# Kernel tuning notes

Hardware: AMD Instinct MI355X
Metric: run time of the kernel (lower is better)

The kernel has to match this reference:

```python
import jax, jax.numpy as jnp
import numpy as np
from functools import partial

EPS = 1e-8

@partial(jax.custom_vjp, nondiff_argnums=(2, 3))
def ste_quantize(x, scale, clamp_min, clamp_max):
    # forward: clamp(round(x/scale), min, max); backward: grad/scale (STE)
    return jnp.clip(jnp.round(x / scale), clamp_min, clamp_max)

def _ste_fwd(x, scale, clamp_min, clamp_max):
    return ste_quantize(x, scale, clamp_min, clamp_max), scale

def _ste_bwd(clamp_min, clamp_max, scale, g):
    return (g / scale, jnp.zeros_like(scale))

ste_quantize.defvjp(_ste_fwd, _ste_bwd)


def setup_inputs() -> dict:
    key = jax.random.key(0)
    kx, kw = jax.random.split(key)
    x = jax.random.normal(kx, (4, 4096, 2048), dtype=jnp.float32)
    # nn.init.normal_(weight, mean=0.0, std=0.006)
    weight = 0.006 * jax.random.normal(kw, (2048, 2048), dtype=jnp.float32)
    return {"x": x, "weight": weight}


def reference(x, weight):
    # per-tensor ternary weight quantization: alpha = mean(|W|)
    alpha = jnp.maximum(jnp.mean(jnp.abs(weight)), EPS)
    w_q = ste_quantize(weight, alpha, -1.0, 1.0)  # (out, in), values in {-1,0,1}
    # per-token int8 activation quantization: beta = max(|x|)/127
    beta = jnp.maximum(jnp.max(jnp.abs(x), axis=-1, keepdims=True) / 127.0, EPS)  # (b,s,1)
    x_q = ste_quantize(x, beta, -127.0, 127.0)  # (b,s,in)
    # fp32 GEMM on quantized values, then dequant rescale
    y = jnp.einsum('bsi,oi->bso', x_q, w_q)
    return y * alpha * beta
```

## Files before the change

kernel.cpp:

```cpp
#include <hip/hip_runtime.h>

#define IN_DIM 2048
#define OUT_DIM 2048
#define EPS 1e-8f

#define BK 128
#define NKT (IN_DIM / BK)
#define HALF 16384

using int32x4 = __attribute__((ext_vector_type(4))) int;

__global__ __launch_bounds__(256) void absum_kernel(const float* __restrict__ w,
                                                    double* __restrict__ sum, int n4) {
    int tid = blockIdx.x * blockDim.x + threadIdx.x;
    int stride = gridDim.x * blockDim.x;
    float s = 0.f;
    for (int i = tid; i < n4; i += stride) {
        float4 v = ((const float4*)w)[i];
        s += fabsf(v.x) + fabsf(v.y) + fabsf(v.z) + fabsf(v.w);
    }
    for (int off = 32; off; off >>= 1) s += __shfl_down(s, off);
    __shared__ float wsum[4];
    int lane = threadIdx.x & 63, wave = threadIdx.x >> 6;
    if (lane == 0) wsum[wave] = s;
    __syncthreads();
    if (threadIdx.x == 0) {
        double t = (double)wsum[0] + (double)wsum[1] + (double)wsum[2] + (double)wsum[3];
        atomicAdd(sum, t);
    }
}

__global__ __launch_bounds__(256) void quantw_kernel(const float* __restrict__ w,
                                                     const double* __restrict__ sumptr,
                                                     signed char* __restrict__ wq,
                                                     float* __restrict__ alpha_out, int n4) {
    float alpha = fmaxf((float)(*sumptr * (1.0 / (double)(IN_DIM * OUT_DIM))), EPS);
    int i = blockIdx.x * blockDim.x + threadIdx.x;
    if (i == 0) *alpha_out = alpha;
    if (i >= n4) return;
    float4 v = ((const float4*)w)[i];
    char4 q;
    q.x = (signed char)fminf(fmaxf(rintf(v.x / alpha), -1.f), 1.f);
    q.y = (signed char)fminf(fmaxf(rintf(v.y / alpha), -1.f), 1.f);
    q.z = (signed char)fminf(fmaxf(rintf(v.z / alpha), -1.f), 1.f);
    q.w = (signed char)fminf(fmaxf(rintf(v.w / alpha), -1.f), 1.f);
    ((char4*)wq)[i] = q;
}

__global__ __launch_bounds__(256) void quantx_kernel(const float* __restrict__ x,
                                                     signed char* __restrict__ xq,
                                                     float* __restrict__ beta_arr,
                                                     int tokens) {
    const int tid = threadIdx.x;
    const int lane = tid & 63, wave = tid >> 6;
    __shared__ float wmax[4];
    for (int t = blockIdx.x; t < tokens; t += gridDim.x) {
        const float4* row = (const float4*)(x + (size_t)t * IN_DIM);
        float4 v0 = row[tid];
        float4 v1 = row[tid + 256];
        float m = fmaxf(fmaxf(fmaxf(fabsf(v0.x), fabsf(v0.y)), fmaxf(fabsf(v0.z), fabsf(v0.w))),
                        fmaxf(fmaxf(fabsf(v1.x), fabsf(v1.y)), fmaxf(fabsf(v1.z), fabsf(v1.w))));
        for (int off = 32; off; off >>= 1) m = fmaxf(m, __shfl_xor(m, off));
        if (lane == 0) wmax[wave] = m;
        __syncthreads();
        m = fmaxf(fmaxf(wmax[0], wmax[1]), fmaxf(wmax[2], wmax[3]));
        float beta = fmaxf(m * (1.f / 127.f), EPS);
        if (tid == 0) beta_arr[t] = beta;
        char4 q0, q1;
        q0.x = (signed char)fminf(fmaxf(rintf(v0.x / beta), -127.f), 127.f);
        q0.y = (signed char)fminf(fmaxf(rintf(v0.y / beta), -127.f), 127.f);
        q0.z = (signed char)fminf(fmaxf(rintf(v0.z / beta), -127.f), 127.f);
        q0.w = (signed char)fminf(fmaxf(rintf(v0.w / beta), -127.f), 127.f);
        q1.x = (signed char)fminf(fmaxf(rintf(v1.x / beta), -127.f), 127.f);
        q1.y = (signed char)fminf(fmaxf(rintf(v1.y / beta), -127.f), 127.f);
        q1.z = (signed char)fminf(fmaxf(rintf(v1.z / beta), -127.f), 127.f);
        q1.w = (signed char)fminf(fmaxf(rintf(v1.w / beta), -127.f), 127.f);
        char4* orow = (char4*)(xq + (size_t)t * IN_DIM);
        orow[tid] = q0;
        orow[tid + 256] = q1;
        __syncthreads();
    }
}

__device__ __forceinline__ void gll(const signed char* g, signed char* l) {
    __builtin_amdgcn_global_load_lds((const __attribute__((address_space(1))) void*)g,
        (__attribute__((address_space(3))) void*)l, 16, 0, 0);
}

#define CLUSTER(BASE, AF)                                                                      \
    __builtin_amdgcn_s_setprio(1);                                                             \
    _Pragma("unroll")                                                                          \
    for (int m_ = 0; m_ < 4; ++m_)                                                             \
        _Pragma("unroll")                                                                      \
        for (int n_ = 0; n_ < 4; ++n_)                                                         \
            acc[(BASE) + m_][n_] = __builtin_amdgcn_mfma_i32_16x16x64_i8(                      \
                AF[m_], bf[n_], acc[(BASE) + m_][n_], 0, 0, 0);                                \
    __builtin_amdgcn_s_setprio(0);

template<bool STG, bool TAIL>
__device__ __forceinline__ void ktile(int T, signed char* lds, int32x4 (&acc)[8][4],
                                      int aoff, int boff, int f0, int f1,
                                      const signed char* a0, const signed char* a1,
                                      const signed char* b0, const signed char* b1) {
    const int s = (T & 1) * HALF;
    const int d = ((T + 1) & 1) * HALF;
    const size_t ko = (size_t)(T + 1) * BK;
    int32x4 af0[4], af1[4], bf[4];

#pragma unroll
    for (int m = 0; m < 4; ++m) af0[m] = *(const int32x4*)(lds + s + aoff + m * 1024);
#pragma unroll
    for (int n = 0; n < 4; ++n) bf[n] = *(const int32x4*)(lds + 65536 + s + boff + n * 1024);
    if constexpr (STG) { gll(a0 + ko, lds + d + f0); gll(a1 + ko, lds + d + f1); }
#pragma unroll
    for (int m = 0; m < 4; ++m) af1[m] = *(const int32x4*)(lds + s + aoff + 4096 + m * 1024);
    CLUSTER(0, af0)
    if constexpr (STG) { gll(b0 + ko, lds + 65536 + d + f0); gll(b1 + ko, lds + 65536 + d + f1); }
    CLUSTER(4, af1)
    if constexpr (TAIL) asm volatile("s_waitcnt vmcnt(0)" ::: "memory");
    else                asm volatile("s_waitcnt vmcnt(4)" ::: "memory");
    __builtin_amdgcn_s_barrier();

#pragma unroll
    for (int m = 0; m < 4; ++m) af0[m] = *(const int32x4*)(lds + 32768 + s + aoff + m * 1024);
#pragma unroll
    for (int n = 0; n < 4; ++n) bf[n] = *(const int32x4*)(lds + 98304 + s + boff + n * 1024);
    if constexpr (STG) { gll(a0 + ko + 64, lds + 32768 + d + f0); gll(a1 + ko + 64, lds + 32768 + d + f1); }
#pragma unroll
    for (int m = 0; m < 4; ++m) af1[m] = *(const int32x4*)(lds + 32768 + s + aoff + 4096 + m * 1024);
    CLUSTER(0, af0)
    if constexpr (STG) { gll(b0 + ko + 64, lds + 98304 + d + f0); gll(b1 + ko + 64, lds + 98304 + d + f1); }
    CLUSTER(4, af1)
    if constexpr (!TAIL) {
        asm volatile("s_waitcnt vmcnt(4)" ::: "memory");
        __builtin_amdgcn_s_barrier();
    }
}

__global__ __launch_bounds__(512, 2) void gemm_kernel(const signed char* __restrict__ xq,
                                                      const signed char* __restrict__ wq,
                                                      const float* __restrict__ beta,
                                                      const float* __restrict__ alpha_p,
                                                      float* __restrict__ out) {
    extern __shared__ signed char lds[];
    const int tid = threadIdx.x;
    const int lane = tid & 63;
    const int wave = tid >> 6;
    const int wm = wave >> 2;
    const int wn = wave & 3;
    const int row0 = blockIdx.x * 256;
    const int col0 = blockIdx.y * 256;

    const int f0 = tid * 16;
    const int f1 = f0 + 8192;
    const int g0 = f0 >> 10, kg0 = (f0 >> 8) & 3, r0 = (f0 >> 4) & 15;
    const int g1 = f1 >> 10, kg1 = (f1 >> 8) & 3, r1 = (f1 >> 4) & 15;
    const signed char* a0 = xq + (size_t)(row0 + g0 * 16 + r0) * IN_DIM + kg0 * 16;
    const signed char* a1 = xq + (size_t)(row0 + g1 * 16 + r1) * IN_DIM + kg1 * 16;
    const signed char* b0 = wq + (size_t)(col0 + g0 * 16 + r0) * IN_DIM + kg0 * 16;
    const signed char* b1 = wq + (size_t)(col0 + g1 * 16 + r1) * IN_DIM + kg1 * 16;

    const int kr = (lane >> 4) * 256 + (lane & 15) * 16;
    const int aoff = wm * 8192 + kr;
    const int boff = wn * 4096 + kr;

    int32x4 acc[8][4] = {};

    gll(a0, lds + f0);              gll(a1, lds + f1);
    gll(b0, lds + 65536 + f0);      gll(b1, lds + 65536 + f1);
    gll(a0 + 64, lds + 32768 + f0); gll(a1 + 64, lds + 32768 + f1);
    gll(b0 + 64, lds + 98304 + f0); gll(b1 + 64, lds + 98304 + f1);
    asm volatile("s_waitcnt vmcnt(4)" ::: "memory");
    __builtin_amdgcn_s_barrier();

    for (int T = 0; T < NKT - 1; ++T)
        ktile<true, false>(T, lds, acc, aoff, boff, f0, f1, a0, a1, b0, b1);
    ktile<false, true>(NKT - 1, lds, acc, aoff, boff, f0, f1, a0, a1, b0, b1);

    const float alpha = *alpha_p;
#pragma unroll
    for (int mi = 0; mi < 8; ++mi) {
        int rbase = row0 + wm * 128 + mi * 16 + ((lane >> 4) << 2);
#pragma unroll
        for (int r = 0; r < 4; ++r) {
            int row = rbase + r;
            float scale = alpha * beta[row];
#pragma unroll
            for (int n = 0; n < 4; ++n) {
                int col = col0 + wn * 64 + n * 16 + (lane & 15);
                out[(size_t)row * OUT_DIM + col] = (float)acc[mi][n][r] * scale;
            }
        }
    }
}

extern "C" void kernel_launch(void* const* d_in, const int* in_sizes, int n_in,
                              void* d_out, int out_size, void* d_ws, size_t ws_size,
                              hipStream_t stream) {
    const float* x = (const float*)d_in[0];
    const float* w = (const float*)d_in[1];
    float* out = (float*)d_out;

    const int tokens = in_sizes[0] / IN_DIM;
    const int n_w = in_sizes[1];
    const int n_w4 = n_w / 4;

    char* ws = (char*)d_ws;
    double* d_sum = (double*)ws;
    float* d_alpha = (float*)(ws + 8);
    float* d_beta = (float*)(ws + 256);
    signed char* d_wq = (signed char*)(ws + 256 + 65536);
    signed char* d_xq = d_wq + (size_t)n_w;

    hipMemsetAsync(d_ws, 0, 16, stream);

    absum_kernel<<<1024, 256, 0, stream>>>(w, d_sum, n_w4);
    quantw_kernel<<<(n_w4 + 255) / 256, 256, 0, stream>>>(w, d_sum, d_wq, d_alpha, n_w4);
    quantx_kernel<<<2048, 256, 0, stream>>>(x, d_xq, d_beta, tokens);

    hipFuncSetAttribute((const void*)gemm_kernel,
                        hipFuncAttributeMaxDynamicSharedMemorySize, 131072);

    dim3 grid(16384 / 256, OUT_DIM / 256);
    gemm_kernel<<<grid, 512, 131072, stream>>>(d_xq, d_wq, d_beta, d_alpha, out);
}
```

Before: 152.4 us.

## Restructure int8 GEMM to 256x128 tiles with triple-buffered BK=64 pipeline

Replaces the 256x256, 512-thread, double-buffered BK=128 GEMM with a 256x128 tile on 256 threads (4 waves, each 128x64). It uses a three-slot LDS ring with BK=64, so loads are issued two tiles ahead and there is one barrier per k-step. LDS drops from 128 KB to 72 KB per block, and the grid now iterates columns fastest so blocks sharing an A row-panel run close together. The aim is better occupancy and latency hiding, at the cost of more k-iterations, halved B reuse per A tile, and more redundant A traffic across column blocks.

```diff
diff --git a/kernel.cpp b/kernel.cpp
--- a/kernel.cpp
+++ b/kernel.cpp
@@ -4,9 +4,12 @@
 #define OUT_DIM 2048
 #define EPS 1e-8f
 
-#define BK 128
-#define NKT (IN_DIM / BK)
-#define HALF 16384
+#define BM 256
+#define BN 128
+#define BK 64
+#define NT (IN_DIM / BK)
+#define SLOT 24576
+#define LDS_SZ 73728
 
 using int32x4 = __attribute__((ext_vector_type(4))) int;
 
@@ -87,57 +90,7 @@
         (__attribute__((address_space(3))) void*)l, 16, 0, 0);
 }
 
-#define CLUSTER(BASE, AF)                                                                      \
-    __builtin_amdgcn_s_setprio(1);                                                             \
-    _Pragma("unroll")                                                                          \
-    for (int m_ = 0; m_ < 4; ++m_)                                                             \
-        _Pragma("unroll")                                                                      \
-        for (int n_ = 0; n_ < 4; ++n_)                                                         \
-            acc[(BASE) + m_][n_] = __builtin_amdgcn_mfma_i32_16x16x64_i8(                      \
-                AF[m_], bf[n_], acc[(BASE) + m_][n_], 0, 0, 0);                                \
-    __builtin_amdgcn_s_setprio(0);
-
-template<bool STG, bool TAIL>
-__device__ __forceinline__ void ktile(int T, signed char* lds, int32x4 (&acc)[8][4],
-                                      int aoff, int boff, int f0, int f1,
-                                      const signed char* a0, const signed char* a1,
-                                      const signed char* b0, const signed char* b1) {
-    const int s = (T & 1) * HALF;
-    const int d = ((T + 1) & 1) * HALF;
-    const size_t ko = (size_t)(T + 1) * BK;
-    int32x4 af0[4], af1[4], bf[4];
-
-#pragma unroll
-    for (int m = 0; m < 4; ++m) af0[m] = *(const int32x4*)(lds + s + aoff + m * 1024);
-#pragma unroll
-    for (int n = 0; n < 4; ++n) bf[n] = *(const int32x4*)(lds + 65536 + s + boff + n * 1024);
-    if constexpr (STG) { gll(a0 + ko, lds + d + f0); gll(a1 + ko, lds + d + f1); }
-#pragma unroll
-    for (int m = 0; m < 4; ++m) af1[m] = *(const int32x4*)(lds + s + aoff + 4096 + m * 1024);
-    CLUSTER(0, af0)
-    if constexpr (STG) { gll(b0 + ko, lds + 65536 + d + f0); gll(b1 + ko, lds + 65536 + d + f1); }
-    CLUSTER(4, af1)
-    if constexpr (TAIL) asm volatile("s_waitcnt vmcnt(0)" ::: "memory");
-    else                asm volatile("s_waitcnt vmcnt(4)" ::: "memory");
-    __builtin_amdgcn_s_barrier();
-
-#pragma unroll
-    for (int m = 0; m < 4; ++m) af0[m] = *(const int32x4*)(lds + 32768 + s + aoff + m * 1024);
-#pragma unroll
-    for (int n = 0; n < 4; ++n) bf[n] = *(const int32x4*)(lds + 98304 + s + boff + n * 1024);
-    if constexpr (STG) { gll(a0 + ko + 64, lds + 32768 + d + f0); gll(a1 + ko + 64, lds + 32768 + d + f1); }
-#pragma unroll
-    for (int m = 0; m < 4; ++m) af1[m] = *(const int32x4*)(lds + 32768 + s + aoff + 4096 + m * 1024);
-    CLUSTER(0, af0)
-    if constexpr (STG) { gll(b0 + ko + 64, lds + 98304 + d + f0); gll(b1 + ko + 64, lds + 98304 + d + f1); }
-    CLUSTER(4, af1)
-    if constexpr (!TAIL) {
-        asm volatile("s_waitcnt vmcnt(4)" ::: "memory");
-        __builtin_amdgcn_s_barrier();
-    }
-}
-
-__global__ __launch_bounds__(512, 2) void gemm_kernel(const signed char* __restrict__ xq,
+__global__ __launch_bounds__(256, 2) void gemm_kernel(const signed char* __restrict__ xq,
                                                       const signed char* __restrict__ wq,
                                                       const float* __restrict__ beta,
                                                       const float* __restrict__ alpha_p,
@@ -146,36 +99,81 @@
     const int tid = threadIdx.x;
     const int lane = tid & 63;
     const int wave = tid >> 6;
-    const int wm = wave >> 2;
-    const int wn = wave & 3;
-    const int row0 = blockIdx.x * 256;
-    const int col0 = blockIdx.y * 256;
-
-    const int f0 = tid * 16;
-    const int f1 = f0 + 8192;
-    const int g0 = f0 >> 10, kg0 = (f0 >> 8) & 3, r0 = (f0 >> 4) & 15;
-    const int g1 = f1 >> 10, kg1 = (f1 >> 8) & 3, r1 = (f1 >> 4) & 15;
-    const signed char* a0 = xq + (size_t)(row0 + g0 * 16 + r0) * IN_DIM + kg0 * 16;
-    const signed char* a1 = xq + (size_t)(row0 + g1 * 16 + r1) * IN_DIM + kg1 * 16;
-    const signed char* b0 = wq + (size_t)(col0 + g0 * 16 + r0) * IN_DIM + kg0 * 16;
-    const signed char* b1 = wq + (size_t)(col0 + g1 * 16 + r1) * IN_DIM + kg1 * 16;
-
-    const int kr = (lane >> 4) * 256 + (lane & 15) * 16;
+    const int wm = wave >> 1;
+    const int wn = wave & 1;
+    const int col0 = blockIdx.x * BN;
+    const int row0 = blockIdx.y * BM;
+
+    const int f = tid * 16;
+    const int srow = ((tid >> 6) << 4) + (tid & 15);
+    const int skg = ((tid >> 4) & 3) << 4;
+    const signed char* aP[4];
+    const signed char* bP[2];
+#pragma unroll
+    for (int c = 0; c < 4; ++c) aP[c] = xq + (size_t)(row0 + srow + 64 * c) * IN_DIM + skg;
+#pragma unroll
+    for (int c = 0; c < 2; ++c) bP[c] = wq + (size_t)(col0 + srow + 64 * c) * IN_DIM + skg;
+
+    const int kr = ((lane >> 4) << 8) + ((lane & 15) << 4);
     const int aoff = wm * 8192 + kr;
-    const int boff = wn * 4096 + kr;
+    const int boff = 16384 + wn * 4096 + kr;
 
     int32x4 acc[8][4] = {};
 
-    gll(a0, lds + f0);              gll(a1, lds + f1);
-    gll(b0, lds + 65536 + f0);      gll(b1, lds + 65536 + f1);
-    gll(a0 + 64, lds + 32768 + f0); gll(a1 + 64, lds + 32768 + f1);
-    gll(b0 + 64, lds + 98304 + f0); gll(b1 + 64, lds + 98304 + f1);
-    asm volatile("s_waitcnt vmcnt(4)" ::: "memory");
+#pragma unroll
+    for (int c = 0; c < 4; ++c) gll(aP[c], lds + f + c * 4096);
+#pragma unroll
+    for (int c = 0; c < 2; ++c) gll(bP[c], lds + 16384 + f + c * 4096);
+#pragma unroll
+    for (int c = 0; c < 4; ++c) gll(aP[c] + BK, lds + SLOT + f + c * 4096);
+#pragma unroll
+    for (int c = 0; c < 2; ++c) gll(bP[c] + BK, lds + SLOT + 16384 + f + c * 4096);
+    asm volatile("s_waitcnt vmcnt(6)" ::: "memory");
     __builtin_amdgcn_s_barrier();
 
-    for (int T = 0; T < NKT - 1; ++T)
-        ktile<true, false>(T, lds, acc, aoff, boff, f0, f1, a0, a1, b0, b1);
-    ktile<false, true>(NKT - 1, lds, acc, aoff, boff, f0, f1, a0, a1, b0, b1);
+    int s = 0, d = 2;
+    for (int T = 0; T < NT; ++T) {
+        const signed char* ls = lds + s * SLOT;
+        signed char* ldst = lds + d * SLOT;
+        int32x4 af[8], bf[4];
+#pragma unroll
+        for (int m = 0; m < 4; ++m) af[m] = *(const int32x4*)(ls + aoff + m * 1024);
+#pragma unroll
+        for (int n = 0; n < 4; ++n) bf[n] = *(const int32x4*)(ls + boff + n * 1024);
+        if (T < NT - 2) {
+            const size_t ko = (size_t)(T + 2) * BK;
+#pragma unroll
+            for (int c = 0; c < 4; ++c) gll(aP[c] + ko, ldst + f + c * 4096);
+        }
+#pragma unroll
+        for (int m = 0; m < 4; ++m) af[4 + m] = *(const int32x4*)(ls + aoff + 4096 + m * 1024);
+        __builtin_amdgcn_s_setprio(1);
+#pragma unroll
+        for (int m = 0; m < 4; ++m)
+#pragma unroll
+            for (int n = 0; n < 4; ++n)
+                acc[m][n] = __builtin_amdgcn_mfma_i32_16x16x64_i8(af[m], bf[n], acc[m][n], 0, 0, 0);
+        __builtin_amdgcn_s_setprio(0);
+        if (T < NT - 2) {
+            const size_t ko = (size_t)(T + 2) * BK;
+#pragma unroll
+            for (int c = 0; c < 2; ++c) gll(bP[c] + ko, ldst + 16384 + f + c * 4096);
+        }
+        __builtin_amdgcn_s_setprio(1);
+#pragma unroll
+        for (int m = 0; m < 4; ++m)
+#pragma unroll
+            for (int n = 0; n < 4; ++n)
+                acc[4 + m][n] = __builtin_amdgcn_mfma_i32_16x16x64_i8(af[4 + m], bf[n], acc[4 + m][n], 0, 0, 0);
+        __builtin_amdgcn_s_setprio(0);
+        if (T < NT - 1) {
+            if (T < NT - 2) asm volatile("s_waitcnt vmcnt(6)" ::: "memory");
+            else            asm volatile("s_waitcnt vmcnt(0)" ::: "memory");
+            __builtin_amdgcn_s_barrier();
+        }
+        s = (s == 2) ? 0 : s + 1;
+        d = (d == 2) ? 0 : d + 1;
+    }
 
     const float alpha = *alpha_p;
 #pragma unroll
@@ -219,8 +217,8 @@
     quantx_kernel<<<2048, 256, 0, stream>>>(x, d_xq, d_beta, tokens);
 
     hipFuncSetAttribute((const void*)gemm_kernel,
-                        hipFuncAttributeMaxDynamicSharedMemorySize, 131072);
-
-    dim3 grid(16384 / 256, OUT_DIM / 256);
-    gemm_kernel<<<grid, 512, 131072, stream>>>(d_xq, d_wq, d_beta, d_alpha, out);
-}
+                        hipFuncAttributeMaxDynamicSharedMemorySize, LDS_SZ);
+
+    dim3 grid(OUT_DIM / BN, tokens / BM);
+    gemm_kernel<<<grid, 256, LDS_SZ, stream>>>(d_xq, d_wq, d_beta, d_alpha, out);
+}
```

After: 172.0 us. +12.8%, slower.

## Restructure int8 GEMM k-tile into barrier-synchronised LDS-load / MFMA phases

Applied to the files above, without the earlier changes.

Each half k-tile is split into two phases. Each phase loads one A fragment set, then runs a block barrier, waits for LDS reads (lgkmcnt) and places a scheduler fence before a 16-MFMA cluster. The second A fragment array is dropped, so A fragments reuse one register set. The aim is to cut register pressure and to make waves alternate between LDS-read and MFMA phases in a ping-pong style. It adds two extra block barriers per half-tile and removes the overlap of A-fragment loads with the previous MFMA cluster, which may stall the matrix pipe.

```diff
diff --git a/kernel.cpp b/kernel.cpp
--- a/kernel.cpp
+++ b/kernel.cpp
@@ -87,7 +87,12 @@
         (__attribute__((address_space(3))) void*)l, 16, 0, 0);
 }
 
-#define CLUSTER(BASE, AF)                                                                      \
+#define PRE_MFMA()                                              \
+    __builtin_amdgcn_s_barrier();                               \
+    asm volatile("s_waitcnt lgkmcnt(0)" ::: "memory");          \
+    __builtin_amdgcn_sched_barrier(0);
+
+#define MFMA16(BASE, AF)                                                                       \
     __builtin_amdgcn_s_setprio(1);                                                             \
     _Pragma("unroll")                                                                          \
     for (int m_ = 0; m_ < 4; ++m_)                                                             \
@@ -105,32 +110,40 @@
     const int s = (T & 1) * HALF;
     const int d = ((T + 1) & 1) * HALF;
     const size_t ko = (size_t)(T + 1) * BK;
-    int32x4 af0[4], af1[4], bf[4];
-
-#pragma unroll
-    for (int m = 0; m < 4; ++m) af0[m] = *(const int32x4*)(lds + s + aoff + m * 1024);
+    int32x4 af[4], bf[4];
+
+#pragma unroll
+    for (int m = 0; m < 4; ++m) af[m] = *(const int32x4*)(lds + s + aoff + m * 1024);
 #pragma unroll
     for (int n = 0; n < 4; ++n) bf[n] = *(const int32x4*)(lds + 65536 + s + boff + n * 1024);
     if constexpr (STG) { gll(a0 + ko, lds + d + f0); gll(a1 + ko, lds + d + f1); }
-#pragma unroll
-    for (int m = 0; m < 4; ++m) af1[m] = *(const int32x4*)(lds + s + aoff + 4096 + m * 1024);
-    CLUSTER(0, af0)
+    PRE_MFMA()
+    MFMA16(0, af)
+    __builtin_amdgcn_s_barrier();
+
+#pragma unroll
+    for (int m = 0; m < 4; ++m) af[m] = *(const int32x4*)(lds + s + aoff + 4096 + m * 1024);
     if constexpr (STG) { gll(b0 + ko, lds + 65536 + d + f0); gll(b1 + ko, lds + 65536 + d + f1); }
-    CLUSTER(4, af1)
+    PRE_MFMA()
+    MFMA16(4, af)
     if constexpr (TAIL) asm volatile("s_waitcnt vmcnt(0)" ::: "memory");
     else                asm volatile("s_waitcnt vmcnt(4)" ::: "memory");
     __builtin_amdgcn_s_barrier();
 
 #pragma unroll
-    for (int m = 0; m < 4; ++m) af0[m] = *(const int32x4*)(lds + 32768 + s + aoff + m * 1024);
+    for (int m = 0; m < 4; ++m) af[m] = *(const int32x4*)(lds + 32768 + s + aoff + m * 1024);
 #pragma unroll
     for (int n = 0; n < 4; ++n) bf[n] = *(const int32x4*)(lds + 98304 + s + boff + n * 1024);
     if constexpr (STG) { gll(a0 + ko + 64, lds + 32768 + d + f0); gll(a1 + ko + 64, lds + 32768 + d + f1); }
-#pragma unroll
-    for (int m = 0; m < 4; ++m) af1[m] = *(const int32x4*)(lds + 32768 + s + aoff + 4096 + m * 1024);
-    CLUSTER(0, af0)
+    PRE_MFMA()
+    MFMA16(0, af)
+    __builtin_amdgcn_s_barrier();
+
+#pragma unroll
+    for (int m = 0; m < 4; ++m) af[m] = *(const int32x4*)(lds + 32768 + s + aoff + 4096 + m * 1024);
     if constexpr (STG) { gll(b0 + ko + 64, lds + 98304 + d + f0); gll(b1 + ko + 64, lds + 98304 + d + f1); }
-    CLUSTER(4, af1)
+    PRE_MFMA()
+    MFMA16(4, af)
     if constexpr (!TAIL) {
         asm volatile("s_waitcnt vmcnt(4)" ::: "memory");
         __builtin_amdgcn_s_barrier();
```

New measurement: 152.7 us. No clear change (+0.2%).
